# Kernel optimization log

Measured on AMD Instinct MI355X. Metric: run time of the kernel, lower is better.

The kernel has to match this reference:

```python
import jax, jax.numpy as jnp
import numpy as np
import itertools

BINS_NUM = 35
BINS_SIZE = 9
ORDERS = (2, 3, 4, 5)

def _comb_idx(n, k):
    # combinations with replacement of indices 0..n-1, shape [ncomb, k]
    return np.array(list(itertools.combinations_with_replacement(range(n), k)), dtype=np.int32)

_COMB = {k: _comb_idx(BINS_SIZE, k) for k in ORDERS}


def setup_inputs() -> dict:
    key = jax.random.key(0)
    x = jax.random.normal(key, (1024, BINS_NUM * BINS_SIZE), dtype=jnp.float32)
    return {"x": x}


def reference(x) -> jnp.ndarray:
    B = x.shape[0]
    bins = x.reshape(B, BINS_NUM, BINS_SIZE)          # [B, 35, 9]
    parts = [bins]                                     # 'origin' slice first
    for k in ORDERS:
        idx = jnp.asarray(_COMB[k])                    # [ncomb_k, k]
        gathered = bins[:, :, idx]                     # [B, 35, ncomb_k, k]
        parts.append(jnp.prod(gathered, axis=-1))      # [B, 35, ncomb_k]
    # per-bin concat [origin, de2, de3, de4, de5], then flatten bins -> matches
    # torch's outer concat over bins since bin is the leading concat axis here.
    out = jnp.concatenate(parts, axis=-1)              # [B, 35, 2001]
    return out.reshape(B, -1)                          # [B, 70035]
```

## Files before the change

### kernel.cpp

```cpp
#include <hip/hip_runtime.h>

#define BSZ 9
#define NPB 2001
#define N2 45
#define N3 165
#define N4 495
#define O2 9
#define O3 54
#define O4 219
#define ONE_SLOT 714
#define LSZ 740

#define WAVE_SYNC() asm volatile("s_waitcnt lgkmcnt(0)" ::: "memory")

__device__ __forceinline__ unsigned sw(unsigned s) { return s + (s >> 5); }
constexpr unsigned csw(unsigned s) { return s + (s >> 5); }

constexpr unsigned pslot2(unsigned i, unsigned j) {
    return O2 + i * 9u - i * (i - 1u) / 2u + (j - i);
}

struct Tabs {
    unsigned short p2[N2];
    unsigned short p3[N3];
    unsigned short p4[N4];
};
constexpr Tabs make_tabs() {
    Tabs t{};
    { int p = 0;
      for (unsigned i = 0; i < 9; ++i)
          for (unsigned j = i; j < 9; ++j)
              t.p2[p++] = (unsigned short)(i | (j << 8)); }
    { int p = 0;
      for (unsigned a = 0; a < 9; ++a)
          for (unsigned b = a; b < 9; ++b) {
              const unsigned ps = pslot2(a, b);
              for (unsigned c = b; c < 9; ++c)
                  t.p3[p++] = (unsigned short)(ps | (c << 8));
          } }
    { int p = 0; unsigned ts = O3;
      for (unsigned a = 0; a < 9; ++a)
          for (unsigned b = a; b < 9; ++b)
              for (unsigned c = b; c < 9; ++c) {
                  for (unsigned d = c; d < 9; ++d)
                      t.p4[p++] = (unsigned short)(ts | (d << 8));
                  ++ts;
              } }
    return t;
}
__constant__ Tabs g_tabs = make_tabs();

struct Full { unsigned t[NPB]; };
constexpr Full make_full() {
    Full f{};
    for (unsigned j = 0; j < ONE_SLOT; ++j)
        f.t[j] = j | (ONE_SLOT << 16);
    { int p = ONE_SLOT; unsigned qs = O4;
      for (unsigned a = 0; a < 9; ++a)
          for (unsigned b = a; b < 9; ++b)
              for (unsigned c = b; c < 9; ++c)
                  for (unsigned d = c; d < 9; ++d) {
                      for (unsigned e = d; e < 9; ++e)
                          f.t[p++] = qs | (e << 16);
                      ++qs;
                  } }
    return f;
}
__constant__ Full g_full = make_full();

__global__ __launch_bounds__(256) void poly_expand_kernel(
        const float* __restrict__ x, float* __restrict__ out, int ntask) {
    __shared__ float L[4][LSZ];
    const int wave = threadIdx.x >> 6;
    const int lane = threadIdx.x & 63;
    const int task = blockIdx.x * 4 + wave;
    if (task >= ntask) return;
    float* Lw = L[wave];

    if (lane < 9)        Lw[sw((unsigned)lane)] = x[(size_t)task * BSZ + lane];
    else if (lane == 9)  Lw[csw(ONE_SLOT)] = 1.0f;
    WAVE_SYNC();

    if (lane < N2) {
        const unsigned pk = g_tabs.p2[lane];
        Lw[sw(O2 + (unsigned)lane)] = Lw[sw(pk & 255u)] * Lw[sw(pk >> 8)];
    }
    WAVE_SYNC();

    #pragma unroll
    for (int k = 0; k < 3; ++k) {
        const int s = lane + 64 * k;
        if (s < N3) {
            const unsigned pk = g_tabs.p3[s];
            Lw[sw(O3 + (unsigned)s)] = Lw[sw(pk & 255u)] * Lw[sw(pk >> 8)];
        }
    }
    WAVE_SYNC();

    #pragma unroll
    for (int k = 0; k < 8; ++k) {
        const int s = lane + 64 * k;
        if (s < N4) {
            const unsigned pk = g_tabs.p4[s];
            Lw[sw(O4 + (unsigned)s)] = Lw[sw(pk & 255u)] * Lw[sw(pk >> 8)];
        }
    }
    WAVE_SYNC();

    const unsigned rb = (unsigned)task * NPB;
    const unsigned h = (unsigned)((4 - (task & 3)) & 3);

    if (lane < (int)h) out[rb + lane] = Lw[sw((unsigned)lane)];

    const unsigned n4 = (NPB - h) >> 2;
    #pragma unroll 2
    for (int k = 0; k < 8; ++k) {
        const unsigned i = (unsigned)lane + 64u * k;
        if (i < n4) {
            const unsigned j0 = h + 4u * i;
            float r[4];
            #pragma unroll
            for (int e = 0; e < 4; ++e) {
                const unsigned pk = g_full.t[j0 + e];
                r[e] = Lw[sw(pk & 0xFFFFu)] * Lw[sw(pk >> 16)];
            }
            *reinterpret_cast<float4*>(out + rb + j0) =
                make_float4(r[0], r[1], r[2], r[3]);
        }
    }

    const unsigned jt = h + 4u * n4;
    if (lane < (int)(NPB - jt)) {
        const unsigned j = jt + (unsigned)lane;
        const unsigned pk = g_full.t[j];
        out[rb + j] = Lw[sw(pk & 0xFFFFu)] * Lw[sw(pk >> 16)];
    }
}

extern "C" void kernel_launch(void* const* d_in, const int* in_sizes, int n_in,
                              void* d_out, int out_size, void* d_ws, size_t ws_size,
                              hipStream_t stream) {
    const float* x = (const float*)d_in[0];
    float* out = (float*)d_out;
    const int ntask = in_sizes[0] / BSZ;
    const int blocks = (ntask + 3) / 4;
    poly_expand_kernel<<<blocks, 256, 0, stream>>>(x, out, ntask);
}
```

Baseline: 61.11 us.

## Persistent waves with register-cached index tables and aligned float4 copy of low-order slots

Turns the kernel into a grid-stride persistent loop, capped at 2048 blocks, where each wave loads its gather tables from constant memory into registers once and reuses them across tasks. The LDS slot layout is shifted by the task's alignment offset so the origin and degree-2..4 slots can be copied straight to the output as aligned float4s. Only the degree-5 products are computed per element, using byte offsets stored in the tables. The LDS bank swizzle is dropped, and register pressure rises from holding 24+ table entries per lane.

Measured after the change: 52.03 us. 14.9% less time.

```diff
diff --git a/kernel.cpp b/kernel.cpp
--- a/kernel.cpp
+++ b/kernel.cpp
@@ -9,22 +9,17 @@
 #define O3 54
 #define O4 219
 #define ONE_SLOT 714
-#define LSZ 740
+#define LSZ 720
+#define NBLOCKS 2048
+#define STRIDE_T (NBLOCKS * 4)
 
 #define WAVE_SYNC() asm volatile("s_waitcnt lgkmcnt(0)" ::: "memory")
-
-__device__ __forceinline__ unsigned sw(unsigned s) { return s + (s >> 5); }
-constexpr unsigned csw(unsigned s) { return s + (s >> 5); }
 
 constexpr unsigned pslot2(unsigned i, unsigned j) {
     return O2 + i * 9u - i * (i - 1u) / 2u + (j - i);
 }
 
-struct Tabs {
-    unsigned short p2[N2];
-    unsigned short p3[N3];
-    unsigned short p4[N4];
-};
+struct Tabs { unsigned short p2[N2]; unsigned short p3[N3]; unsigned short p4[N4]; };
 constexpr Tabs make_tabs() {
     Tabs t{};
     { int p = 0;
@@ -54,14 +49,14 @@
 constexpr Full make_full() {
     Full f{};
     for (unsigned j = 0; j < ONE_SLOT; ++j)
-        f.t[j] = j | (ONE_SLOT << 16);
+        f.t[j] = (4u * j) | ((4u * ONE_SLOT) << 16);
     { int p = ONE_SLOT; unsigned qs = O4;
       for (unsigned a = 0; a < 9; ++a)
           for (unsigned b = a; b < 9; ++b)
               for (unsigned c = b; c < 9; ++c)
                   for (unsigned d = c; d < 9; ++d) {
                       for (unsigned e = d; e < 9; ++e)
-                          f.t[p++] = qs | (e << 16);
+                          f.t[p++] = (4u * qs) | ((4u * e) << 16);
                       ++qs;
                   } }
     return f;
@@ -73,67 +68,88 @@
     __shared__ float L[4][LSZ];
     const int wave = threadIdx.x >> 6;
     const int lane = threadIdx.x & 63;
-    const int task = blockIdx.x * 4 + wave;
-    if (task >= ntask) return;
-    float* Lw = L[wave];
+    const int w0 = blockIdx.x * 4 + wave;
+    if (w0 >= ntask) return;
+    float* const Lw = L[wave];
 
-    if (lane < 9)        Lw[sw((unsigned)lane)] = x[(size_t)task * BSZ + lane];
-    else if (lane == 9)  Lw[csw(ONE_SLOT)] = 1.0f;
-    WAVE_SYNC();
+    const unsigned o     = (unsigned)w0 & 3u;
+    const unsigned a     = (4u - o) & 3u;
+    const unsigned mA    = (ONE_SLOT - a) >> 2;
+    const unsigned mB0   = (ONE_SLOT - a + 3u) >> 2;
+    const unsigned Mfull = (NPB - a) >> 2;
+    float* const Ls = Lw + o;
+    const char* const Lc = (const char*)Ls;
+    const float4* const Af4 = (const float4*)(Lw + o + a);
 
-    if (lane < N2) {
-        const unsigned pk = g_tabs.p2[lane];
-        Lw[sw(O2 + (unsigned)lane)] = Lw[sw(pk & 255u)] * Lw[sw(pk >> 8)];
-    }
-    WAVE_SYNC();
+    const unsigned t2 = (lane < N2) ? (unsigned)g_tabs.p2[lane] : 0u;
+    unsigned t3[3], t4[8];
+    #pragma unroll
+    for (int k = 0; k < 3; ++k) { const int s = lane + 64 * k;
+        t3[k] = (s < N3) ? (unsigned)g_tabs.p3[s] : 0u; }
+    #pragma unroll
+    for (int k = 0; k < 8; ++k) { const int s = lane + 64 * k;
+        t4[k] = (s < N4) ? (unsigned)g_tabs.p4[s] : 0u; }
 
+    const unsigned jb0 = a + 4u * mB0;
+    unsigned bpk[6][4];
     #pragma unroll
-    for (int k = 0; k < 3; ++k) {
-        const int s = lane + 64 * k;
-        if (s < N3) {
-            const unsigned pk = g_tabs.p3[s];
-            Lw[sw(O3 + (unsigned)s)] = Lw[sw(pk & 255u)] * Lw[sw(pk >> 8)];
-        }
-    }
-    WAVE_SYNC();
-
-    #pragma unroll
-    for (int k = 0; k < 8; ++k) {
-        const int s = lane + 64 * k;
-        if (s < N4) {
-            const unsigned pk = g_tabs.p4[s];
-            Lw[sw(O4 + (unsigned)s)] = Lw[sw(pk & 255u)] * Lw[sw(pk >> 8)];
-        }
-    }
-    WAVE_SYNC();
-
-    const unsigned rb = (unsigned)task * NPB;
-    const unsigned h = (unsigned)((4 - (task & 3)) & 3);
-
-    if (lane < (int)h) out[rb + lane] = Lw[sw((unsigned)lane)];
-
-    const unsigned n4 = (NPB - h) >> 2;
-    #pragma unroll 2
-    for (int k = 0; k < 8; ++k) {
-        const unsigned i = (unsigned)lane + 64u * k;
-        if (i < n4) {
-            const unsigned j0 = h + 4u * i;
-            float r[4];
-            #pragma unroll
-            for (int e = 0; e < 4; ++e) {
-                const unsigned pk = g_full.t[j0 + e];
-                r[e] = Lw[sw(pk & 0xFFFFu)] * Lw[sw(pk >> 16)];
-            }
-            *reinterpret_cast<float4*>(out + rb + j0) =
-                make_float4(r[0], r[1], r[2], r[3]);
-        }
+    for (int k = 0; k < 6; ++k) {
+        const unsigned idx = (unsigned)lane + 64u * k;
+        #pragma unroll
+        for (int e = 0; e < 4; ++e)
+            bpk[k][e] = (idx < 321u) ? g_full.t[jb0 + 4u * idx + (unsigned)e] : 0u;
     }
 
-    const unsigned jt = h + 4u * n4;
-    if (lane < (int)(NPB - jt)) {
-        const unsigned j = jt + (unsigned)lane;
-        const unsigned pk = g_full.t[j];
-        out[rb + j] = Lw[sw(pk & 0xFFFFu)] * Lw[sw(pk >> 16)];
+    const unsigned z1s = a + 4u * mA, z1n = 4u * (mB0 - mA);
+    const unsigned z2s = a + 4u * Mfull, z2n = (unsigned)NPB - z2s;
+    int jm = -1;
+    if ((unsigned)lane < a)                 jm = lane;
+    else if ((unsigned)lane < a + z1n)      jm = (int)(z1s + ((unsigned)lane - a));
+    else if ((unsigned)lane < a + z1n + z2n) jm = (int)(z2s + ((unsigned)lane - a - z1n));
+    const unsigned mpk = (jm >= 0) ? g_full.t[jm] : 0u;
+
+    for (int task = w0; task < ntask; task += STRIDE_T) {
+        const unsigned rb = (unsigned)task * (unsigned)NPB;
+        WAVE_SYNC();
+
+        if (lane < 9)       Ls[lane] = x[(size_t)task * BSZ + lane];
+        else if (lane == 9) Ls[ONE_SLOT] = 1.0f;
+        WAVE_SYNC();
+        if (lane < N2) Ls[O2 + lane] = Ls[t2 & 255u] * Ls[t2 >> 8];
+        WAVE_SYNC();
+        #pragma unroll
+        for (int k = 0; k < 3; ++k) { const int s = lane + 64 * k;
+            if (s < N3) Ls[O3 + s] = Ls[t3[k] & 255u] * Ls[t3[k] >> 8]; }
+        WAVE_SYNC();
+        #pragma unroll
+        for (int k = 0; k < 8; ++k) { const int s = lane + 64 * k;
+            if (s < N4) Ls[O4 + s] = Ls[t4[k] & 255u] * Ls[t4[k] >> 8]; }
+        WAVE_SYNC();
+
+        float4* const po4 = (float4*)(out + rb + a);
+
+        #pragma unroll
+        for (int k = 0; k < 3; ++k) {
+            const unsigned m = (unsigned)lane + 64u * k;
+            if (m < mA) po4[m] = Af4[m];
+        }
+        #pragma unroll
+        for (int k = 0; k < 6; ++k) {
+            const unsigned idx = (unsigned)lane + 64u * k;
+            if (idx < 321u) {
+                float r[4];
+                #pragma unroll
+                for (int e = 0; e < 4; ++e) {
+                    const unsigned pk = bpk[k][e];
+                    r[e] = *(const float*)(Lc + (pk & 0xFFFFu)) *
+                           *(const float*)(Lc + (pk >> 16));
+                }
+                po4[mB0 + idx] = make_float4(r[0], r[1], r[2], r[3]);
+            }
+        }
+        if (jm >= 0)
+            out[rb + (unsigned)jm] = *(const float*)(Lc + (mpk & 0xFFFFu)) *
+                                     *(const float*)(Lc + (mpk >> 16));
     }
 }
 
@@ -143,6 +159,7 @@
     const float* x = (const float*)d_in[0];
     float* out = (float*)d_out;
     const int ntask = in_sizes[0] / BSZ;
-    const int blocks = (ntask + 3) / 4;
+    int blocks = (ntask + 3) / 4;
+    if (blocks > NBLOCKS) blocks = NBLOCKS;
     poly_expand_kernel<<<blocks, 256, 0, stream>>>(x, out, ntask);
 }
```
